# Kernel tuning notes

Measured on AMD Instinct MI355X. Metric: run time of the kernel, lower is better.

Reference implementation:

```python
import jax, jax.numpy as jnp
import numpy as np

N_NODES = 50000
N_EDGES = 800000
IN_F = 128
HID = 64
HEADS = 4
OUT_F = 16
NEG_SLOPE = 0.2
BN_EPS = 1e-5


def setup_inputs() -> dict:
    key = jax.random.key(0)
    ks = jax.random.split(key, 16)
    g = lambda k, s: (jax.random.normal(k, s, dtype=jnp.float32) * 0.05)
    inp = {
        'x': jax.random.normal(ks[0], (N_NODES, IN_F), dtype=jnp.float32),
        'edge_index': jax.random.randint(ks[1], (2, N_EDGES), 0, N_NODES, dtype=jnp.int64),
        # layer 1: GATConv(128 -> 64, heads=4, concat)
        'W1': g(ks[2], (IN_F, HEADS * HID)),
        'as1': g(ks[3], (HEADS, HID)), 'ad1': g(ks[4], (HEADS, HID)),
        'b1': jnp.zeros((HEADS * HID,), jnp.float32),
        'g1': jnp.ones((HEADS * HID,), jnp.float32), 'be1': jnp.zeros((HEADS * HID,), jnp.float32),
        'm1': jnp.zeros((HEADS * HID,), jnp.float32), 'v1': jnp.ones((HEADS * HID,), jnp.float32),
        # layer 2: GATConv(256 -> 64, heads=4, concat)
        'W2': g(ks[5], (HEADS * HID, HEADS * HID)),
        'as2': g(ks[6], (HEADS, HID)), 'ad2': g(ks[7], (HEADS, HID)),
        'b2': jnp.zeros((HEADS * HID,), jnp.float32),
        'g2': jnp.ones((HEADS * HID,), jnp.float32), 'be2': jnp.zeros((HEADS * HID,), jnp.float32),
        'm2': jnp.zeros((HEADS * HID,), jnp.float32), 'v2': jnp.ones((HEADS * HID,), jnp.float32),
        # layer 3: GATConv(256 -> 16, heads=1, concat=False)
        'W3': g(ks[8], (HEADS * HID, OUT_F)),
        'as3': g(ks[9], (1, OUT_F)), 'ad3': g(ks[10], (1, OUT_F)),
        'b3': jnp.zeros((OUT_F,), jnp.float32),
    }
    return inp


def gat_conv(x, src, dst, W, a_src, a_dst, b, concat):
    n = x.shape[0]
    H, C = a_src.shape
    h = (x @ W).reshape(n, H, C)                       # [N,H,C]
    s_node = jnp.sum(h * a_src[None], axis=-1)         # [N,H]
    d_node = jnp.sum(h * a_dst[None], axis=-1)         # [N,H]
    e = jax.nn.leaky_relu(s_node[src] + d_node[dst], NEG_SLOPE)   # [E,H]
    # segment softmax over incoming edges of each dst node
    e_max = jax.ops.segment_max(e, dst, num_segments=n)
    e_exp = jnp.exp(e - e_max[dst])
    denom = jax.ops.segment_sum(e_exp, dst, num_segments=n)
    alpha = e_exp / denom[dst]                         # [E,H]
    msg = h[src] * alpha[:, :, None]                   # [E,H,C]
    out = jax.ops.segment_sum(msg, dst, num_segments=n)  # [N,H,C]
    out = out.reshape(n, H * C) if concat else out.mean(axis=1)
    return out + b


def batchnorm(x, gamma, beta, mean, var):
    return (x - mean) * jax.lax.rsqrt(var + BN_EPS) * gamma + beta


def reference(x, edge_index, W1, as1, ad1, b1, g1, be1, m1, v1,
              W2, as2, ad2, b2, g2, be2, m2, v2, W3, as3, ad3, b3):
    n = x.shape[0]
    loops = jnp.arange(n, dtype=edge_index.dtype)
    src = jnp.concatenate([edge_index[0], loops])      # PyG add_self_loops
    dst = jnp.concatenate([edge_index[1], loops])
    h = gat_conv(x, src, dst, W1, as1, ad1, b1, concat=True)
    h = jax.nn.relu(batchnorm(h, g1, be1, m1, v1))
    h = gat_conv(h, src, dst, W2, as2, ad2, b2, concat=True)
    h = jax.nn.relu(batchnorm(h, g2, be2, m2, v2))
    out = gat_conv(h, src, dst, W3, as3, ad3, b3, concat=False)
    return out  # out_channels=16 != 1 -> no sigmoid
```

## Files before the change

kernel.cpp:

```cpp
#include <hip/hip_runtime.h>
#include <math.h>

#define NN 50000
#define NE 800000
#define ET (NE + NN)
#define F1 256
#define NEG 0.2f
#define BN_EPS 1e-5f

typedef __attribute__((ext_vector_type(8))) short short8;
typedef __attribute__((ext_vector_type(4))) float float4v;
typedef __attribute__((ext_vector_type(4))) unsigned short ushort4v;

__device__ __forceinline__ float bf2f(unsigned short u) {
    unsigned int x = ((unsigned int)u) << 16;
    return __builtin_bit_cast(float, x);
}
__device__ __forceinline__ unsigned short f2bf(float f) {
    unsigned int x = __builtin_bit_cast(unsigned int, f);
    unsigned int lsb = (x >> 16) & 1u;
    x += 0x7fffu + lsb;
    return (unsigned short)(x >> 16);
}
__device__ __forceinline__ float lrelu(float x) { return x > 0.f ? x : NEG * x; }

__device__ __forceinline__ void gl_lds16(const unsigned short* g, unsigned short* l) {
    __builtin_amdgcn_global_load_lds((const __attribute__((address_space(1))) void*)g,
                                     (__attribute__((address_space(3))) void*)l, 16, 0, 0);
}

__global__ void cast_f32_bf16(const float* __restrict__ in, unsigned short* __restrict__ out, int n4) {
    int i = (blockIdx.x * 256 + threadIdx.x);
    if (i < n4) {
        float4 v = ((const float4*)in)[i];
        ushort4 o;
        o.x = f2bf(v.x); o.y = f2bf(v.y); o.z = f2bf(v.z); o.w = f2bf(v.w);
        ((ushort4*)out)[i] = o;
    }
}

__global__ void prep_misc(const float* __restrict__ W1, unsigned short* __restrict__ W1t,
                          const float* __restrict__ W2, unsigned short* __restrict__ W2t,
                          const float* __restrict__ b1, const float* __restrict__ g1,
                          const float* __restrict__ be1, const float* __restrict__ m1,
                          const float* __restrict__ v1, float* __restrict__ S1, float* __restrict__ T1,
                          const float* __restrict__ b2, const float* __restrict__ g2,
                          const float* __restrict__ be2, const float* __restrict__ m2,
                          const float* __restrict__ v2, float* __restrict__ S2, float* __restrict__ T2) {
    int blk = blockIdx.x, tid = threadIdx.x;
    if (blk < 128) {
        int id = blk * 256 + tid;
        int n = id >> 7, k = id & 127;
        W1t[id] = f2bf(W1[k * 256 + n]);
    } else if (blk < 384) {
        int id = (blk - 128) * 256 + tid;
        int n = id >> 8, k = id & 255;
        W2t[id] = f2bf(W2[k * 256 + n]);
    } else if (blk == 384) {
        float s = g1[tid] * rsqrtf(v1[tid] + BN_EPS);
        S1[tid] = s;
        T1[tid] = (b1[tid] - m1[tid]) * s + be1[tid];
    } else {
        float s = g2[tid] * rsqrtf(v2[tid] + BN_EPS);
        S2[tid] = s;
        T2[tid] = (b2[tid] - m2[tid]) * s + be2[tid];
    }
}

__global__ void edge_hist_rank(const int* __restrict__ ei, int* __restrict__ counts, int* __restrict__ rank) {
    int e = blockIdx.x * 256 + threadIdx.x;
    if (e < ET) {
        int dst = (e < NE) ? ei[NE + e] : (e - NE);
        rank[e] = atomicAdd(&counts[dst], 1);
    }
}

__global__ void scan_a(const int* __restrict__ counts, int* __restrict__ rowptr, int* __restrict__ bsum) {
    __shared__ int s[256];
    int t = threadIdx.x, i = blockIdx.x * 256 + t;
    int v = (i < NN) ? counts[i] : 0;
    s[t] = v;
    __syncthreads();
    for (int off = 1; off < 256; off <<= 1) {
        int add = (t >= off) ? s[t - off] : 0;
        __syncthreads();
        s[t] += add;
        __syncthreads();
    }
    if (i < NN) rowptr[i + 1] = s[t];
    if (t == 255) bsum[blockIdx.x] = s[255];
}

__global__ void scan_b(int* __restrict__ bsum, int nb) {
    __shared__ int s[256];
    int t = threadIdx.x;
    int v = (t < nb) ? bsum[t] : 0;
    s[t] = v;
    __syncthreads();
    for (int off = 1; off < 256; off <<= 1) {
        int add = (t >= off) ? s[t - off] : 0;
        __syncthreads();
        s[t] += add;
        __syncthreads();
    }
    if (t < nb) bsum[t] = s[t] - v;
}

__global__ void scan_c(int* __restrict__ rowptr, const int* __restrict__ bsum) {
    int i = blockIdx.x * 256 + threadIdx.x;
    if (i < NN) rowptr[i + 1] += bsum[i >> 8];
    if (i == 0) rowptr[0] = 0;
}

__global__ void edge_place(const int* __restrict__ ei, const int* __restrict__ rowptr,
                           const int* __restrict__ rank, int* __restrict__ csr) {
    int e = blockIdx.x * 256 + threadIdx.x;
    if (e < ET) {
        int src, dst;
        if (e < NE) { src = ei[e]; dst = ei[NE + e]; }
        else        { src = e - NE; dst = src; }
        csr[rowptr[dst] + rank[e]] = src;
    }
}

template<int K>
__global__ __launch_bounds__(256, 3) void gemm_lds(const unsigned short* __restrict__ A,
                                                   const unsigned short* __restrict__ Bt,
                                                   unsigned short* __restrict__ C,
                                                   const float* __restrict__ a_s,
                                                   const float* __restrict__ a_d,
                                                   float* __restrict__ s_arr,
                                                   float* __restrict__ d_arr,
                                                   int M) {
    __shared__ __align__(16) unsigned short As[128 * 64];
    __shared__ __align__(16) unsigned short Bs[128 * 64];
    int tid = threadIdx.x, lane = tid & 63, w = tid >> 6;
    int wr = w >> 1, wc = w & 1;
    int mBase = blockIdx.x * 128, nBase = blockIdx.y * 128;
    int lm = lane & 15, q = lane >> 4;

    float4v acc[4][4];
    for (int i = 0; i < 4; ++i)
        for (int j = 0; j < 4; ++j)
            acc[i][j] = (float4v){0.f, 0.f, 0.f, 0.f};

    const unsigned short* Ap[4];
    const unsigned short* Bp[4];
    for (int p = 0; p < 4; ++p) {
        int slot = p * 256 + tid;
        int row = slot >> 3;
        int csrc = (slot & 7) ^ (row & 7);
        int gm = mBase + row; if (gm >= M) gm = M - 1;
        Ap[p] = A + (size_t)gm * K + csrc * 8;
        Bp[p] = Bt + (size_t)(nBase + row) * K + csrc * 8;
    }

    for (int k0 = 0; k0 < K; k0 += 64) {
        #pragma unroll
        for (int p = 0; p < 4; ++p)
            gl_lds16(Ap[p] + k0, As + ((size_t)p * 256 + w * 64) * 8);
        #pragma unroll
        for (int p = 0; p < 4; ++p)
            gl_lds16(Bp[p] + k0, Bs + ((size_t)p * 256 + w * 64) * 8);
        __syncthreads();
        #pragma unroll
        for (int ks = 0; ks < 64; ks += 32) {
            int cb = ks >> 3;
            short8 af[4], bfr[4];
            #pragma unroll
            for (int i = 0; i < 4; ++i) {
                int row = wr * 64 + i * 16 + lm;
                int ch = (cb + q) ^ (row & 7);
                af[i] = *(const short8*)(As + row * 64 + ch * 8);
            }
            #pragma unroll
            for (int j = 0; j < 4; ++j) {
                int row = wc * 64 + j * 16 + lm;
                int ch = (cb + q) ^ (row & 7);
                bfr[j] = *(const short8*)(Bs + row * 64 + ch * 8);
            }
            #pragma unroll
            for (int i = 0; i < 4; ++i)
                #pragma unroll
                for (int j = 0; j < 4; ++j)
                    acc[i][j] = __builtin_amdgcn_mfma_f32_16x16x32_bf16(af[i], bfr[j], acc[i][j], 0, 0, 0);
        }
        __syncthreads();
    }

    for (int i = 0; i < 4; ++i)
        for (int j = 0; j < 4; ++j) {
            int col = nBase + wc * 64 + j * 16 + lm;
            for (int r = 0; r < 4; ++r) {
                int row = mBase + wr * 64 + i * 16 + q * 4 + r;
                if (row < M) C[(size_t)row * 256 + col] = f2bf(acc[i][j][r]);
            }
        }
    int head = blockIdx.y * 2 + wc;
    float as_j[4], ad_j[4];
    for (int j = 0; j < 4; ++j) {
        as_j[j] = a_s[head * 64 + j * 16 + lm];
        ad_j[j] = a_d[head * 64 + j * 16 + lm];
    }
    for (int i = 0; i < 4; ++i)
        for (int r = 0; r < 4; ++r) {
            float sp = acc[i][0][r] * as_j[0] + acc[i][1][r] * as_j[1]
                     + acc[i][2][r] * as_j[2] + acc[i][3][r] * as_j[3];
            float dp = acc[i][0][r] * ad_j[0] + acc[i][1][r] * ad_j[1]
                     + acc[i][2][r] * ad_j[2] + acc[i][3][r] * ad_j[3];
            for (int off = 1; off < 16; off <<= 1) {
                sp += __shfl_xor(sp, off);
                dp += __shfl_xor(dp, off);
            }
            int row = mBase + wr * 64 + i * 16 + q * 4 + r;
            if (lm == 0 && row < M) {
                s_arr[row * 4 + head] = sp;
                d_arr[row * 4 + head] = dp;
            }
        }
}

__global__ __launch_bounds__(256) void agg12(const unsigned short* __restrict__ h,
                                             const float* __restrict__ s_arr, const float* __restrict__ d_arr,
                                             const int* __restrict__ rowptr, const int* __restrict__ csr,
                                             const float* __restrict__ S, const float* __restrict__ T,
                                             unsigned short* __restrict__ out) {
    __shared__ float wls[4][64 * 5];
    int lane = threadIdx.x & 63;
    int wv = threadIdx.x >> 6;
    int node = blockIdx.x * 4 + wv;
    if (node >= NN) return;
    int r0 = rowptr[node], r1 = rowptr[node + 1];
    float4 dv = *(const float4*)(d_arr + node * 4);
    float* wbuf = &wls[wv][0];
    int lp = lane & 31;
    int half = lane >> 5;
    int head8 = lp >> 3;
    const unsigned short* hbase = h + lp * 8;

    float acc[8] = {0.f, 0.f, 0.f, 0.f, 0.f, 0.f, 0.f, 0.f};
    float den0 = 0.f, den1 = 0.f, den2 = 0.f, den3 = 0.f;

    for (int base = r0; base < r1; base += 64) {
        int cnt = min(64, r1 - base);
        if (lane < cnt) {
            int src = csr[base + lane];
            float4 sv = *(const float4*)(s_arr + src * 4);
            float w0 = __expf(lrelu(sv.x + dv.x));
            float w1 = __expf(lrelu(sv.y + dv.y));
            float w2 = __expf(lrelu(sv.z + dv.z));
            float w3 = __expf(lrelu(sv.w + dv.w));
            den0 += w0; den1 += w1; den2 += w2; den3 += w3;
            float* wp = wbuf + lane * 5;
            wp[0] = w0; wp[1] = w1; wp[2] = w2; wp[3] = w3;
            wp[4] = __int_as_float(src);
        } else if (lane == cnt) {
            float* wp = wbuf + lane * 5;
            wp[0] = 0.f; wp[1] = 0.f; wp[2] = 0.f; wp[3] = 0.f;
            wp[4] = __int_as_float(node);
        }
        int cpad = (cnt + 1) & ~1;
        for (int k = 0; k < cpad; k += 2) {
            int k2 = k + half;
            const float* wp = wbuf + k2 * 5;
            int src = __float_as_int(wp[4]);
            float wgt = wp[head8];
            short8 hv = *(const short8*)(hbase + (size_t)src * F1);
            acc[0] += wgt * bf2f((unsigned short)hv[0]);
            acc[1] += wgt * bf2f((unsigned short)hv[1]);
            acc[2] += wgt * bf2f((unsigned short)hv[2]);
            acc[3] += wgt * bf2f((unsigned short)hv[3]);
            acc[4] += wgt * bf2f((unsigned short)hv[4]);
            acc[5] += wgt * bf2f((unsigned short)hv[5]);
            acc[6] += wgt * bf2f((unsigned short)hv[6]);
            acc[7] += wgt * bf2f((unsigned short)hv[7]);
        }
    }
    for (int u = 0; u < 8; ++u) acc[u] += __shfl_xor(acc[u], 32);
    for (int off = 32; off; off >>= 1) {
        den0 += __shfl_xor(den0, off);
        den1 += __shfl_xor(den1, off);
        den2 += __shfl_xor(den2, off);
        den3 += __shfl_xor(den3, off);
    }
    if (half == 0) {
        float den = (head8 == 0) ? den0 : (head8 == 1) ? den1 : (head8 == 2) ? den2 : den3;
        float inv = 1.f / den;
        int j = lp * 8;
        float4 Sv0 = *(const float4*)(S + j);
        float4 Sv1 = *(const float4*)(S + j + 4);
        float4 Tv0 = *(const float4*)(T + j);
        float4 Tv1 = *(const float4*)(T + j + 4);
        short8 o;
        o[0] = (short)f2bf(fmaxf(acc[0] * inv * Sv0.x + Tv0.x, 0.f));
        o[1] = (short)f2bf(fmaxf(acc[1] * inv * Sv0.y + Tv0.y, 0.f));
        o[2] = (short)f2bf(fmaxf(acc[2] * inv * Sv0.z + Tv0.z, 0.f));
        o[3] = (short)f2bf(fmaxf(acc[3] * inv * Sv0.w + Tv0.w, 0.f));
        o[4] = (short)f2bf(fmaxf(acc[4] * inv * Sv1.x + Tv1.x, 0.f));
        o[5] = (short)f2bf(fmaxf(acc[5] * inv * Sv1.y + Tv1.y, 0.f));
        o[6] = (short)f2bf(fmaxf(acc[6] * inv * Sv1.z + Tv1.z, 0.f));
        o[7] = (short)f2bf(fmaxf(acc[7] * inv * Sv1.w + Tv1.w, 0.f));
        *(short8*)(out + (size_t)node * F1 + j) = o;
    }
}

__global__ __launch_bounds__(256) void gemm3_sd(const unsigned short* __restrict__ A,
                                                const float* __restrict__ W3,
                                                const float* __restrict__ as3, const float* __restrict__ ad3,
                                                float* __restrict__ h3, float* __restrict__ s3, float* __restrict__ d3) {
    __shared__ __align__(16) float Ws[256 * 16];
    int tid = threadIdx.x;
    for (int p = tid; p < 1024; p += 256)
        ((float4*)Ws)[p] = ((const float4*)W3)[p];
    __syncthreads();
    int nl = tid >> 2;
    int q = tid & 3;
    int node = blockIdx.x * 64 + nl;
    float acc[16];
    for (int j = 0; j < 16; ++j) acc[j] = 0.f;
    if (node < NN) {
        const unsigned short* ar = A + (size_t)node * F1;
        for (int c = q; c < 32; c += 4) {
            short8 v8 = *(const short8*)(ar + c * 8);
            for (int u = 0; u < 8; ++u) {
                float av = bf2f((unsigned short)v8[u]);
                const float* wr = Ws + (c * 8 + u) * 16;
                float4 w0 = *(const float4*)(wr);
                float4 w1 = *(const float4*)(wr + 4);
                float4 w2 = *(const float4*)(wr + 8);
                float4 w3 = *(const float4*)(wr + 12);
                acc[0]  += av * w0.x; acc[1]  += av * w0.y; acc[2]  += av * w0.z; acc[3]  += av * w0.w;
                acc[4]  += av * w1.x; acc[5]  += av * w1.y; acc[6]  += av * w1.z; acc[7]  += av * w1.w;
                acc[8]  += av * w2.x; acc[9]  += av * w2.y; acc[10] += av * w2.z; acc[11] += av * w2.w;
                acc[12] += av * w3.x; acc[13] += av * w3.y; acc[14] += av * w3.z; acc[15] += av * w3.w;
            }
        }
    }
    for (int j = 0; j < 16; ++j) {
        acc[j] += __shfl_xor(acc[j], 1);
        acc[j] += __shfl_xor(acc[j], 2);
    }
    if (q == 0 && node < NN) {
        float sv = 0.f, dvv = 0.f;
        for (int j = 0; j < 16; ++j) {
            h3[(size_t)node * 16 + j] = acc[j];
            sv += acc[j] * as3[j];
            dvv += acc[j] * ad3[j];
        }
        s3[node] = sv;
        d3[node] = dvv;
    }
}

__global__ __launch_bounds__(256) void agg3(const float* __restrict__ h3, const float* __restrict__ s3,
                                            const float* __restrict__ d3, const int* __restrict__ rowptr,
                                            const int* __restrict__ csr, const float* __restrict__ b3,
                                            float* __restrict__ out) {
    int lane = threadIdx.x & 63;
    int node = blockIdx.x * 4 + (threadIdx.x >> 6);
    if (node >= NN) return;
    int r0 = rowptr[node], r1 = rowptr[node + 1];
    float dv = d3[node];
    int c = lane & 15, g = lane >> 4;
    float acc = 0.f, den = 0.f;
    for (int e = r0 + g; e < r1; e += 4) {
        int src = csr[e];
        float w = __expf(lrelu(s3[src] + dv));
        den += w;
        acc += w * h3[(size_t)src * 16 + c];
    }
    acc += __shfl_xor(acc, 16); acc += __shfl_xor(acc, 32);
    den += __shfl_xor(den, 16); den += __shfl_xor(den, 32);
    if (lane < 16) out[(size_t)node * 16 + lane] = acc / den + b3[lane];
}

extern "C" void kernel_launch(void* const* d_in, const int* in_sizes, int n_in,
                              void* d_out, int out_size, void* d_ws, size_t ws_size,
                              hipStream_t stream) {
    const float* x   = (const float*)d_in[0];
    const int*   ei  = (const int*)d_in[1];
    const float* W1  = (const float*)d_in[2];
    const float* as1 = (const float*)d_in[3];
    const float* ad1 = (const float*)d_in[4];
    const float* b1  = (const float*)d_in[5];
    const float* g1  = (const float*)d_in[6];
    const float* be1 = (const float*)d_in[7];
    const float* m1  = (const float*)d_in[8];
    const float* v1  = (const float*)d_in[9];
    const float* W2  = (const float*)d_in[10];
    const float* as2 = (const float*)d_in[11];
    const float* ad2 = (const float*)d_in[12];
    const float* b2  = (const float*)d_in[13];
    const float* g2  = (const float*)d_in[14];
    const float* be2 = (const float*)d_in[15];
    const float* m2  = (const float*)d_in[16];
    const float* v2  = (const float*)d_in[17];
    const float* W3  = (const float*)d_in[18];
    const float* as3 = (const float*)d_in[19];
    const float* ad3 = (const float*)d_in[20];
    const float* b3  = (const float*)d_in[21];

    char* w = (char*)d_ws;
    size_t off = 0;
    auto alloc = [&](size_t bytes) -> void* {
        off = (off + 255) & ~(size_t)255;
        void* p = w + off;
        off += bytes;
        return p;
    };
    unsigned short* xb   = (unsigned short*)alloc((size_t)NN * 128 * 2);
    unsigned short* W1t  = (unsigned short*)alloc(256 * 128 * 2);
    unsigned short* W2t  = (unsigned short*)alloc(256 * 256 * 2);
    unsigned short* Abuf = (unsigned short*)alloc((size_t)NN * F1 * 2);
    unsigned short* Bbuf = (unsigned short*)alloc((size_t)NN * F1 * 2);
    float* h3    = (float*)alloc((size_t)NN * 16 * 4);
    float* s_arr = (float*)alloc((size_t)NN * 4 * 4);
    float* d_arr = (float*)alloc((size_t)NN * 4 * 4);
    float* s3    = (float*)alloc((size_t)NN * 4);
    float* d3    = (float*)alloc((size_t)NN * 4);
    int* counts  = (int*)alloc((size_t)NN * 4);
    int* rowptr  = (int*)alloc((size_t)(NN + 1) * 4);
    int* rank    = (int*)alloc((size_t)ET * 4);
    int* csr     = (int*)alloc((size_t)ET * 4);
    int* bsum    = (int*)alloc(256 * 4);
    float* S1 = (float*)alloc(F1 * 4);
    float* T1 = (float*)alloc(F1 * 4);
    float* S2 = (float*)alloc(F1 * 4);
    float* T2 = (float*)alloc(F1 * 4);
    float* outp = (float*)d_out;

    int nb_scan = (NN + 255) / 256;
    int nb_edge = (ET + 255) / 256;

    cast_f32_bf16<<<(NN * 128 / 4 + 255) / 256, 256, 0, stream>>>(x, xb, NN * 128 / 4);
    prep_misc<<<386, 256, 0, stream>>>(W1, W1t, W2, W2t,
                                       b1, g1, be1, m1, v1, S1, T1,
                                       b2, g2, be2, m2, v2, S2, T2);

    hipMemsetAsync(counts, 0, (size_t)NN * 4, stream);
    edge_hist_rank<<<nb_edge, 256, 0, stream>>>(ei, counts, rank);
    scan_a<<<nb_scan, 256, 0, stream>>>(counts, rowptr, bsum);
    scan_b<<<1, 256, 0, stream>>>(bsum, nb_scan);
    scan_c<<<nb_scan, 256, 0, stream>>>(rowptr, bsum);
    edge_place<<<nb_edge, 256, 0, stream>>>(ei, rowptr, rank, csr);

    dim3 ggrid((NN + 127) / 128, 2);
    int agrid = (NN + 3) / 4;

    gemm_lds<128><<<ggrid, 256, 0, stream>>>(xb, W1t, Abuf, as1, ad1, s_arr, d_arr, NN);
    agg12<<<agrid, 256, 0, stream>>>(Abuf, s_arr, d_arr, rowptr, csr, S1, T1, Bbuf);

    gemm_lds<256><<<ggrid, 256, 0, stream>>>(Bbuf, W2t, Abuf, as2, ad2, s_arr, d_arr, NN);
    agg12<<<agrid, 256, 0, stream>>>(Abuf, s_arr, d_arr, rowptr, csr, S2, T2, Bbuf);

    gemm3_sd<<<(NN + 63) / 64, 256, 0, stream>>>(Bbuf, W3, as3, ad3, h3, s3, d3);
    agg3<<<agrid, 256, 0, stream>>>(h3, s3, d3, rowptr, csr, b3, outp);
}
```

Baseline: 395.7 us.

## Store layer-1 features in fp8, use MFMA for layer-3 GEMM, merge prep kernels

Layer-1 GEMM now writes its output as fp8, and a new fp8 aggregation kernel gathers half as many bytes per edge, which targets the bandwidth-bound neighbour gather. The layer-3 projection moves from a scalar FMA loop to MFMA bf16, with W3 split into hi and lo bf16 halves to keep accuracy close to fp32. The cast, edge histogram and weight prep kernels are merged into one launch to cut launch overhead. Using fp8 for the layer-1 features lowers precision and may push results past the accuracy tolerance.

```diff
diff --git a/kernel.cpp b/kernel.cpp
--- a/kernel.cpp
+++ b/kernel.cpp
@@ -10,6 +10,7 @@
 
 typedef __attribute__((ext_vector_type(8))) short short8;
 typedef __attribute__((ext_vector_type(4))) float float4v;
+typedef __attribute__((ext_vector_type(2))) float float2v;
 typedef __attribute__((ext_vector_type(4))) unsigned short ushort4v;
 
 __device__ __forceinline__ float bf2f(unsigned short u) {
@@ -22,6 +23,10 @@
     x += 0x7fffu + lsb;
     return (unsigned short)(x >> 16);
 }
+__device__ __forceinline__ unsigned char f2fp8(float f) {
+    int p = __builtin_amdgcn_cvt_pk_fp8_f32(f, f, 0, false);
+    return (unsigned char)(p & 0xff);
+}
 __device__ __forceinline__ float lrelu(float x) { return x > 0.f ? x : NEG * x; }
 
 __device__ __forceinline__ void gl_lds16(const unsigned short* g, unsigned short* l) {
@@ -29,34 +34,47 @@
                                      (__attribute__((address_space(3))) void*)l, 16, 0, 0);
 }
 
-__global__ void cast_f32_bf16(const float* __restrict__ in, unsigned short* __restrict__ out, int n4) {
-    int i = (blockIdx.x * 256 + threadIdx.x);
-    if (i < n4) {
-        float4 v = ((const float4*)in)[i];
+__global__ void prep_all(const float* __restrict__ x, unsigned short* __restrict__ xb,
+                         const int* __restrict__ ei, int* __restrict__ counts, int* __restrict__ rank,
+                         const float* __restrict__ W1, unsigned short* __restrict__ W1t,
+                         const float* __restrict__ W2, unsigned short* __restrict__ W2t,
+                         const float* __restrict__ W3, unsigned short* __restrict__ W3h,
+                         unsigned short* __restrict__ W3l,
+                         const float* __restrict__ b1, const float* __restrict__ g1,
+                         const float* __restrict__ be1, const float* __restrict__ m1,
+                         const float* __restrict__ v1, float* __restrict__ S1, float* __restrict__ T1,
+                         const float* __restrict__ b2, const float* __restrict__ g2,
+                         const float* __restrict__ be2, const float* __restrict__ m2,
+                         const float* __restrict__ v2, float* __restrict__ S2, float* __restrict__ T2) {
+    int blk = blockIdx.x, tid = threadIdx.x;
+    if (blk < 6250) {
+        int i = blk * 256 + tid;
+        float4 v = ((const float4*)x)[i];
         ushort4 o;
         o.x = f2bf(v.x); o.y = f2bf(v.y); o.z = f2bf(v.z); o.w = f2bf(v.w);
-        ((ushort4*)out)[i] = o;
-    }
-}
-
-__global__ void prep_misc(const float* __restrict__ W1, unsigned short* __restrict__ W1t,
-                          const float* __restrict__ W2, unsigned short* __restrict__ W2t,
-                          const float* __restrict__ b1, const float* __restrict__ g1,
-                          const float* __restrict__ be1, const float* __restrict__ m1,
-                          const float* __restrict__ v1, float* __restrict__ S1, float* __restrict__ T1,
-                          const float* __restrict__ b2, const float* __restrict__ g2,
-                          const float* __restrict__ be2, const float* __restrict__ m2,
-                          const float* __restrict__ v2, float* __restrict__ S2, float* __restrict__ T2) {
-    int blk = blockIdx.x, tid = threadIdx.x;
-    if (blk < 128) {
-        int id = blk * 256 + tid;
+        ((ushort4*)xb)[i] = o;
+    } else if (blk < 9571) {
+        int e = (blk - 6250) * 256 + tid;
+        if (e < ET) {
+            int dst = (e < NE) ? ei[NE + e] : (e - NE);
+            rank[e] = atomicAdd(&counts[dst], 1);
+        }
+    } else if (blk < 9699) {
+        int id = (blk - 9571) * 256 + tid;
         int n = id >> 7, k = id & 127;
         W1t[id] = f2bf(W1[k * 256 + n]);
-    } else if (blk < 384) {
-        int id = (blk - 128) * 256 + tid;
+    } else if (blk < 9955) {
+        int id = (blk - 9699) * 256 + tid;
         int n = id >> 8, k = id & 255;
         W2t[id] = f2bf(W2[k * 256 + n]);
-    } else if (blk == 384) {
+    } else if (blk < 9971) {
+        int id = (blk - 9955) * 256 + tid;
+        int n = id >> 8, k = id & 255;
+        float v = W3[k * 16 + n];
+        unsigned short hi = f2bf(v);
+        W3h[id] = hi;
+        W3l[id] = f2bf(v - bf2f(hi));
+    } else if (blk == 9971) {
         float s = g1[tid] * rsqrtf(v1[tid] + BN_EPS);
         S1[tid] = s;
         T1[tid] = (b1[tid] - m1[tid]) * s + be1[tid];
@@ -64,14 +82,6 @@
         float s = g2[tid] * rsqrtf(v2[tid] + BN_EPS);
         S2[tid] = s;
         T2[tid] = (b2[tid] - m2[tid]) * s + be2[tid];
-    }
-}
-
-__global__ void edge_hist_rank(const int* __restrict__ ei, int* __restrict__ counts, int* __restrict__ rank) {
-    int e = blockIdx.x * 256 + threadIdx.x;
-    if (e < ET) {
-        int dst = (e < NE) ? ei[NE + e] : (e - NE);
-        rank[e] = atomicAdd(&counts[dst], 1);
     }
 }
 
@@ -123,10 +133,10 @@
     }
 }
 
-template<int K>
+template<int K, bool F8OUT>
 __global__ __launch_bounds__(256, 3) void gemm_lds(const unsigned short* __restrict__ A,
                                                    const unsigned short* __restrict__ Bt,
-                                                   unsigned short* __restrict__ C,
+                                                   void* __restrict__ Cout,
                                                    const float* __restrict__ a_s,
                                                    const float* __restrict__ a_d,
                                                    float* __restrict__ s_arr,
@@ -193,7 +203,12 @@
             int col = nBase + wc * 64 + j * 16 + lm;
             for (int r = 0; r < 4; ++r) {
                 int row = mBase + wr * 64 + i * 16 + q * 4 + r;
-                if (row < M) C[(size_t)row * 256 + col] = f2bf(acc[i][j][r]);
+                if (row < M) {
+                    if constexpr (F8OUT)
+                        ((unsigned char*)Cout)[(size_t)row * 256 + col] = f2fp8(acc[i][j][r]);
+                    else
+                        ((unsigned short*)Cout)[(size_t)row * 256 + col] = f2bf(acc[i][j][r]);
+                }
             }
         }
     int head = blockIdx.y * 2 + wc;
@@ -220,11 +235,11 @@
         }
 }
 
-__global__ __launch_bounds__(256) void agg12(const unsigned short* __restrict__ h,
-                                             const float* __restrict__ s_arr, const float* __restrict__ d_arr,
-                                             const int* __restrict__ rowptr, const int* __restrict__ csr,
-                                             const float* __restrict__ S, const float* __restrict__ T,
-                                             unsigned short* __restrict__ out) {
+__global__ __launch_bounds__(256) void agg12_f8(const unsigned char* __restrict__ h8,
+                                                const float* __restrict__ s_arr, const float* __restrict__ d_arr,
+                                                const int* __restrict__ rowptr, const int* __restrict__ csr,
+                                                const float* __restrict__ S, const float* __restrict__ T,
+                                                unsigned short* __restrict__ out) {
     __shared__ float wls[4][64 * 5];
     int lane = threadIdx.x & 63;
     int wv = threadIdx.x >> 6;
@@ -236,9 +251,9 @@
     int lp = lane & 31;
     int half = lane >> 5;
     int head8 = lp >> 3;
-    const unsigned short* hbase = h + lp * 8;
-
-    float acc[8] = {0.f, 0.f, 0.f, 0.f, 0.f, 0.f, 0.f, 0.f};
+    const unsigned char* hbase = h8 + lp * 8;
+
+    float2v a01 = {0.f, 0.f}, a23 = {0.f, 0.f}, a45 = {0.f, 0.f}, a67 = {0.f, 0.f};
     float den0 = 0.f, den1 = 0.f, den2 = 0.f, den3 = 0.f;
 
     for (int base = r0; base < r1; base += 64) {
@@ -261,21 +276,22 @@
         }
         int cpad = (cnt + 1) & ~1;
         for (int k = 0; k < cpad; k += 2) {
-            int k2 = k + half;
-            const float* wp = wbuf + k2 * 5;
+            const float* wp = wbuf + (k + half) * 5;
             int src = __float_as_int(wp[4]);
             float wgt = wp[head8];
-            short8 hv = *(const short8*)(hbase + (size_t)src * F1);
-            acc[0] += wgt * bf2f((unsigned short)hv[0]);
-            acc[1] += wgt * bf2f((unsigned short)hv[1]);
-            acc[2] += wgt * bf2f((unsigned short)hv[2]);
-            acc[3] += wgt * bf2f((unsigned short)hv[3]);
-            acc[4] += wgt * bf2f((unsigned short)hv[4]);
-            acc[5] += wgt * bf2f((unsigned short)hv[5]);
-            acc[6] += wgt * bf2f((unsigned short)hv[6]);
-            acc[7] += wgt * bf2f((unsigned short)hv[7]);
-        }
-    }
+            uint2 hv = *(const uint2*)(hbase + (size_t)src * 256);
+            float2v c0 = __builtin_amdgcn_cvt_pk_f32_fp8((int)hv.x, false);
+            float2v c1 = __builtin_amdgcn_cvt_pk_f32_fp8((int)hv.x, true);
+            float2v c2 = __builtin_amdgcn_cvt_pk_f32_fp8((int)hv.y, false);
+            float2v c3 = __builtin_amdgcn_cvt_pk_f32_fp8((int)hv.y, true);
+            float2v w2v = {wgt, wgt};
+            a01 += w2v * c0;
+            a23 += w2v * c1;
+            a45 += w2v * c2;
+            a67 += w2v * c3;
+        }
+    }
+    float acc[8] = {a01.x, a01.y, a23.x, a23.y, a45.x, a45.y, a67.x, a67.y};
     for (int u = 0; u < 8; ++u) acc[u] += __shfl_xor(acc[u], 32);
     for (int off = 32; off; off >>= 1) {
         den0 += __shfl_xor(den0, off);
@@ -304,51 +320,122 @@
     }
 }
 
-__global__ __launch_bounds__(256) void gemm3_sd(const unsigned short* __restrict__ A,
-                                                const float* __restrict__ W3,
-                                                const float* __restrict__ as3, const float* __restrict__ ad3,
-                                                float* __restrict__ h3, float* __restrict__ s3, float* __restrict__ d3) {
-    __shared__ __align__(16) float Ws[256 * 16];
-    int tid = threadIdx.x;
-    for (int p = tid; p < 1024; p += 256)
-        ((float4*)Ws)[p] = ((const float4*)W3)[p];
-    __syncthreads();
-    int nl = tid >> 2;
-    int q = tid & 3;
-    int node = blockIdx.x * 64 + nl;
-    float acc[16];
-    for (int j = 0; j < 16; ++j) acc[j] = 0.f;
-    if (node < NN) {
-        const unsigned short* ar = A + (size_t)node * F1;
-        for (int c = q; c < 32; c += 4) {
-            short8 v8 = *(const short8*)(ar + c * 8);
-            for (int u = 0; u < 8; ++u) {
-                float av = bf2f((unsigned short)v8[u]);
-                const float* wr = Ws + (c * 8 + u) * 16;
-                float4 w0 = *(const float4*)(wr);
-                float4 w1 = *(const float4*)(wr + 4);
-                float4 w2 = *(const float4*)(wr + 8);
-                float4 w3 = *(const float4*)(wr + 12);
-                acc[0]  += av * w0.x; acc[1]  += av * w0.y; acc[2]  += av * w0.z; acc[3]  += av * w0.w;
-                acc[4]  += av * w1.x; acc[5]  += av * w1.y; acc[6]  += av * w1.z; acc[7]  += av * w1.w;
-                acc[8]  += av * w2.x; acc[9]  += av * w2.y; acc[10] += av * w2.z; acc[11] += av * w2.w;
-                acc[12] += av * w3.x; acc[13] += av * w3.y; acc[14] += av * w3.z; acc[15] += av * w3.w;
-            }
-        }
-    }
-    for (int j = 0; j < 16; ++j) {
-        acc[j] += __shfl_xor(acc[j], 1);
-        acc[j] += __shfl_xor(acc[j], 2);
-    }
-    if (q == 0 && node < NN) {
-        float sv = 0.f, dvv = 0.f;
-        for (int j = 0; j < 16; ++j) {
-            h3[(size_t)node * 16 + j] = acc[j];
-            sv += acc[j] * as3[j];
-            dvv += acc[j] * ad3[j];
-        }
-        s3[node] = sv;
-        d3[node] = dvv;
+__global__ __launch_bounds__(256) void agg12(const unsigned short* __restrict__ h,
+                                             const float* __restrict__ s_arr, const float* __restrict__ d_arr,
+                                             const int* __restrict__ rowptr, const int* __restrict__ csr,
+                                             const float* __restrict__ S, const float* __restrict__ T,
+                                             unsigned short* __restrict__ out) {
+    __shared__ float wls[4][64 * 5];
+    int lane = threadIdx.x & 63;
+    int wv = threadIdx.x >> 6;
+    int node = blockIdx.x * 4 + wv;
+    if (node >= NN) return;
+    int r0 = rowptr[node], r1 = rowptr[node + 1];
+    float4 dv = *(const float4*)(d_arr + node * 4);
+    float* wbuf = &wls[wv][0];
+    int lp = lane & 31;
+    int half = lane >> 5;
+    int head8 = lp >> 3;
+    const unsigned short* hbase = h + lp * 8;
+
+    float acc[8] = {0.f, 0.f, 0.f, 0.f, 0.f, 0.f, 0.f, 0.f};
+    float den0 = 0.f, den1 = 0.f, den2 = 0.f, den3 = 0.f;
+
+    for (int base = r0; base < r1; base += 64) {
+        int cnt = min(64, r1 - base);
+        if (lane < cnt) {
+            int src = csr[base + lane];
+            float4 sv = *(const float4*)(s_arr + src * 4);
+            float w0 = __expf(lrelu(sv.x + dv.x));
+            float w1 = __expf(lrelu(sv.y + dv.y));
+            float w2 = __expf(lrelu(sv.z + dv.z));
+            float w3 = __expf(lrelu(sv.w + dv.w));
+            den0 += w0; den1 += w1; den2 += w2; den3 += w3;
+            float* wp = wbuf + lane * 5;
+            wp[0] = w0; wp[1] = w1; wp[2] = w2; wp[3] = w3;
+            wp[4] = __int_as_float(src);
+        } else if (lane == cnt) {
+            float* wp = wbuf + lane * 5;
+            wp[0] = 0.f; wp[1] = 0.f; wp[2] = 0.f; wp[3] = 0.f;
+            wp[4] = __int_as_float(node);
+        }
+        int cpad = (cnt + 1) & ~1;
+        for (int k = 0; k < cpad; k += 2) {
+            const float* wp = wbuf + (k + half) * 5;
+            int src = __float_as_int(wp[4]);
+            float wgt = wp[head8];
+            short8 hv = *(const short8*)(hbase + (size_t)src * F1);
+            acc[0] += wgt * bf2f((unsigned short)hv[0]);
+            acc[1] += wgt * bf2f((unsigned short)hv[1]);
+            acc[2] += wgt * bf2f((unsigned short)hv[2]);
+            acc[3] += wgt * bf2f((unsigned short)hv[3]);
+            acc[4] += wgt * bf2f((unsigned short)hv[4]);
+            acc[5] += wgt * bf2f((unsigned short)hv[5]);
+            acc[6] += wgt * bf2f((unsigned short)hv[6]);
+            acc[7] += wgt * bf2f((unsigned short)hv[7]);
+        }
+    }
+    for (int u = 0; u < 8; ++u) acc[u] += __shfl_xor(acc[u], 32);
+    for (int off = 32; off; off >>= 1) {
+        den0 += __shfl_xor(den0, off);
+        den1 += __shfl_xor(den1, off);
+        den2 += __shfl_xor(den2, off);
+        den3 += __shfl_xor(den3, off);
+    }
+    if (half == 0) {
+        float den = (head8 == 0) ? den0 : (head8 == 1) ? den1 : (head8 == 2) ? den2 : den3;
+        float inv = 1.f / den;
+        int j = lp * 8;
+        float4 Sv0 = *(const float4*)(S + j);
+        float4 Sv1 = *(const float4*)(S + j + 4);
+        float4 Tv0 = *(const float4*)(T + j);
+        float4 Tv1 = *(const float4*)(T + j + 4);
+        short8 o;
+        o[0] = (short)f2bf(fmaxf(acc[0] * inv * Sv0.x + Tv0.x, 0.f));
+        o[1] = (short)f2bf(fmaxf(acc[1] * inv * Sv0.y + Tv0.y, 0.f));
+        o[2] = (short)f2bf(fmaxf(acc[2] * inv * Sv0.z + Tv0.z, 0.f));
+        o[3] = (short)f2bf(fmaxf(acc[3] * inv * Sv0.w + Tv0.w, 0.f));
+        o[4] = (short)f2bf(fmaxf(acc[4] * inv * Sv1.x + Tv1.x, 0.f));
+        o[5] = (short)f2bf(fmaxf(acc[5] * inv * Sv1.y + Tv1.y, 0.f));
+        o[6] = (short)f2bf(fmaxf(acc[6] * inv * Sv1.z + Tv1.z, 0.f));
+        o[7] = (short)f2bf(fmaxf(acc[7] * inv * Sv1.w + Tv1.w, 0.f));
+        *(short8*)(out + (size_t)node * F1 + j) = o;
+    }
+}
+
+__global__ __launch_bounds__(256) void gemm3_mfma(const unsigned short* __restrict__ A,
+                                                  const unsigned short* __restrict__ W3h,
+                                                  const unsigned short* __restrict__ W3l,
+                                                  const float* __restrict__ as3, const float* __restrict__ ad3,
+                                                  float* __restrict__ h3, float* __restrict__ s3,
+                                                  float* __restrict__ d3, int M) {
+    int tid = threadIdx.x, lane = tid & 63, w = tid >> 6;
+    int mBase = blockIdx.x * 64 + w * 16;
+    int lm = lane & 15, q = lane >> 4;
+    int row = mBase + lm;
+    int rc = (row < M) ? row : (M - 1);
+    const unsigned short* pA = A + (size_t)rc * 256 + q * 8;
+    const unsigned short* pH = W3h + lm * 256 + q * 8;
+    const unsigned short* pL = W3l + lm * 256 + q * 8;
+    float4v acc = (float4v){0.f, 0.f, 0.f, 0.f};
+    #pragma unroll
+    for (int s = 0; s < 8; ++s) {
+        short8 a  = *(const short8*)(pA + s * 32);
+        short8 bh = *(const short8*)(pH + s * 32);
+        short8 bl = *(const short8*)(pL + s * 32);
+        acc = __builtin_amdgcn_mfma_f32_16x16x32_bf16(a, bh, acc, 0, 0, 0);
+        acc = __builtin_amdgcn_mfma_f32_16x16x32_bf16(a, bl, acc, 0, 0, 0);
+    }
+    float a_s = as3[lm], a_d = ad3[lm];
+    for (int r = 0; r < 4; ++r) {
+        int rw = mBase + q * 4 + r;
+        if (rw < M) h3[(size_t)rw * 16 + lm] = acc[r];
+        float sp = acc[r] * a_s, dp = acc[r] * a_d;
+        for (int off = 1; off < 16; off <<= 1) {
+            sp += __shfl_xor(sp, off);
+            dp += __shfl_xor(dp, off);
+        }
+        if (lm == 0 && rw < M) { s3[rw] = sp; d3[rw] = dp; }
     }
 }
 
@@ -408,11 +495,14 @@
         off += bytes;
         return p;
     };
-    unsigned short* xb   = (unsigned short*)alloc((size_t)NN * 128 * 2);
-    unsigned short* W1t  = (unsigned short*)alloc(256 * 128 * 2);
-    unsigned short* W2t  = (unsigned short*)alloc(256 * 256 * 2);
-    unsigned short* Abuf = (unsigned short*)alloc((size_t)NN * F1 * 2);
-    unsigned short* Bbuf = (unsigned short*)alloc((size_t)NN * F1 * 2);
+    unsigned short* xb    = (unsigned short*)alloc((size_t)NN * 128 * 2);
+    unsigned short* W1t   = (unsigned short*)alloc(256 * 128 * 2);
+    unsigned short* W2t   = (unsigned short*)alloc(256 * 256 * 2);
+    unsigned short* W3h   = (unsigned short*)alloc(16 * 256 * 2);
+    unsigned short* W3l   = (unsigned short*)alloc(16 * 256 * 2);
+    unsigned char*  Abuf8 = (unsigned char*)alloc((size_t)NN * F1);
+    unsigned short* Abuf  = (unsigned short*)alloc((size_t)NN * F1 * 2);
+    unsigned short* Bbuf  = (unsigned short*)alloc((size_t)NN * F1 * 2);
     float* h3    = (float*)alloc((size_t)NN * 16 * 4);
     float* s_arr = (float*)alloc((size_t)NN * 4 * 4);
     float* d_arr = (float*)alloc((size_t)NN * 4 * 4);
@@ -432,13 +522,11 @@
     int nb_scan = (NN + 255) / 256;
     int nb_edge = (ET + 255) / 256;
 
-    cast_f32_bf16<<<(NN * 128 / 4 + 255) / 256, 256, 0, stream>>>(x, xb, NN * 128 / 4);
-    prep_misc<<<386, 256, 0, stream>>>(W1, W1t, W2, W2t,
+    hipMemsetAsync(counts, 0, (size_t)NN * 4, stream);
+    prep_all<<<9973, 256, 0, stream>>>(x, xb, ei, counts, rank,
+                                       W1, W1t, W2, W2t, W3, W3h, W3l,
                                        b1, g1, be1, m1, v1, S1, T1,
                                        b2, g2, be2, m2, v2, S2, T2);
-
-    hipMemsetAsync(counts, 0, (size_t)NN * 4, stream);
-    edge_hist_rank<<<nb_edge, 256, 0, stream>>>(ei, counts, rank);
     scan_a<<<nb_scan, 256, 0, stream>>>(counts, rowptr, bsum);
     scan_b<<<1, 256, 0, stream>>>(bsum, nb_scan);
     scan_c<<<nb_scan, 256, 0, stream>>>(rowptr, bsum);
@@ -447,12 +535,12 @@
     dim3 ggrid((NN + 127) / 128, 2);
     int agrid = (NN + 3) / 4;
 
-    gemm_lds<128><<<ggrid, 256, 0, stream>>>(xb, W1t, Abuf, as1, ad1, s_arr, d_arr, NN);
-    agg12<<<agrid, 256, 0, stream>>>(Abuf, s_arr, d_arr, rowptr, csr, S1, T1, Bbuf);
-
-    gemm_lds<256><<<ggrid, 256, 0, stream>>>(Bbuf, W2t, Abuf, as2, ad2, s_arr, d_arr, NN);
+    gemm_lds<128, true><<<ggrid, 256, 0, stream>>>(xb, W1t, Abuf8, as1, ad1, s_arr, d_arr, NN);
+    agg12_f8<<<agrid, 256, 0, stream>>>(Abuf8, s_arr, d_arr, rowptr, csr, S1, T1, Bbuf);
+
+    gemm_lds<256, false><<<ggrid, 256, 0, stream>>>(Bbuf, W2t, Abuf, as2, ad2, s_arr, d_arr, NN);
     agg12<<<agrid, 256, 0, stream>>>(Abuf, s_arr, d_arr, rowptr, csr, S2, T2, Bbuf);
 
-    gemm3_sd<<<(NN + 63) / 64, 256, 0, stream>>>(Bbuf, W3, as3, ad3, h3, s3, d3);
+    gemm3_mfma<<<(NN + 63) / 64, 256, 0, stream>>>(Bbuf, W3h, W3l, as3, ad3, h3, s3, d3, NN);
     agg3<<<agrid, 256, 0, stream>>>(h3, s3, d3, rowptr, csr, b3, outp);
 }
```

Result: faster. 356.0 us (-10.0%).
